# Kernel optimization log

Measured on AMD Instinct MI355X. Metric: run time of the kernel, lower is better.

Reference implementation:

```python
import jax, jax.numpy as jnp
import numpy as np

DIM, HEADS, DHEAD, CTX_DIM, DFF = 1280, 20, 64, 768, 5120
EPS = 1e-5
SCALE = DHEAD ** -0.5


def layer_norm(x, g, b):
    mu = jnp.mean(x, axis=-1, keepdims=True)
    var = jnp.mean(jnp.square(x - mu), axis=-1, keepdims=True)
    return (x - mu) * jax.lax.rsqrt(var + EPS) * g + b


def cross_attention(x, ctx, wq, wk, wv, wo, bo):
    B, N, _ = x.shape
    M = ctx.shape[1]
    q = jnp.einsum('bne,ef->bnf', x, wq).reshape(B, N, HEADS, DHEAD).transpose(0, 2, 1, 3)
    k = jnp.einsum('bme,ef->bmf', ctx, wk).reshape(B, M, HEADS, DHEAD).transpose(0, 2, 1, 3)
    v = jnp.einsum('bme,ef->bmf', ctx, wv).reshape(B, M, HEADS, DHEAD).transpose(0, 2, 1, 3)
    scores = jnp.einsum('bhnd,bhmd->bhnm', q, k) * SCALE
    attn = jax.nn.softmax(scores, axis=-1)
    out = jnp.einsum('bhnm,bhmd->bhnd', attn, v)
    out = out.transpose(0, 2, 1, 3).reshape(B, N, HEADS * DHEAD)
    return jnp.einsum('bnf,fe->bne', out, wo) + bo


def geglu_ff(x, w1, b1, w2, b2):
    h = jnp.einsum('bne,ef->bnf', x, w1) + b1  # [B,N,2*DFF]
    a, gate = h[..., :DFF], h[..., DFF:]
    h = a * jax.nn.gelu(gate)
    return jnp.einsum('bnf,fe->bne', h, w2) + b2


def block_forward(x, context,
                  g1, be1, wq1, wk1, wv1, wo1, bo1,
                  g2, be2, wq2, wk2, wv2, wo2, bo2,
                  g3, be3, w_ff1, b_ff1, w_ff2, b_ff2):
    x = cross_attention(layer_norm(x, g1, be1), layer_norm(x, g1, be1), wq1, wk1, wv1, wo1, bo1) + x
    x = cross_attention(layer_norm(x, g2, be2), context, wq2, wk2, wv2, wo2, bo2) + x
    return geglu_ff(layer_norm(x, g3, be3), w_ff1, b_ff1, w_ff2, b_ff2) + x


def setup_inputs() -> dict:
    key = jax.random.key(0)
    ks = jax.random.split(key, 20)
    s = 0.02
    inner = HEADS * DHEAD
    return {
        'x': jax.random.normal(ks[0], (4, 1024, DIM), jnp.float32),
        'context': jax.random.normal(ks[1], (4, 77, CTX_DIM), jnp.float32),
        'g1': jnp.ones((DIM,), jnp.float32), 'be1': jnp.zeros((DIM,), jnp.float32),
        'wq1': jax.random.normal(ks[2], (DIM, inner), jnp.float32) * s,
        'wk1': jax.random.normal(ks[3], (DIM, inner), jnp.float32) * s,
        'wv1': jax.random.normal(ks[4], (DIM, inner), jnp.float32) * s,
        'wo1': jax.random.normal(ks[5], (inner, DIM), jnp.float32) * s,
        'bo1': jnp.zeros((DIM,), jnp.float32),
        'g2': jnp.ones((DIM,), jnp.float32), 'be2': jnp.zeros((DIM,), jnp.float32),
        'wq2': jax.random.normal(ks[6], (DIM, inner), jnp.float32) * s,
        'wk2': jax.random.normal(ks[7], (CTX_DIM, inner), jnp.float32) * s,
        'wv2': jax.random.normal(ks[8], (CTX_DIM, inner), jnp.float32) * s,
        'wo2': jax.random.normal(ks[9], (inner, DIM), jnp.float32) * s,
        'bo2': jnp.zeros((DIM,), jnp.float32),
        'g3': jnp.ones((DIM,), jnp.float32), 'be3': jnp.zeros((DIM,), jnp.float32),
        'w_ff1': jax.random.normal(ks[10], (DIM, 2 * DFF), jnp.float32) * s,
        'b_ff1': jnp.zeros((2 * DFF,), jnp.float32),
        'w_ff2': jax.random.normal(ks[11], (DFF, DIM), jnp.float32) * s,
        'b_ff2': jnp.zeros((DIM,), jnp.float32),
    }


def reference(x, context,
              g1, be1, wq1, wk1, wv1, wo1, bo1,
              g2, be2, wq2, wk2, wv2, wo2, bo2,
              g3, be3, w_ff1, b_ff1, w_ff2, b_ff2):
    return block_forward(x, context,
                         g1, be1, wq1, wk1, wv1, wo1, bo1,
                         g2, be2, wq2, wk2, wv2, wo2, bo2,
                         g3, be3, w_ff1, b_ff1, w_ff2, b_ff2)
```

## Files before the change

### kernel.cpp

```cpp
#include <hip/hip_runtime.h>

typedef unsigned short u16;
typedef __bf16 bf16x8 __attribute__((ext_vector_type(8)));
typedef float f32x4 __attribute__((ext_vector_type(4)));

static __device__ __forceinline__ float bf2f(u16 u) {
    union { unsigned int i; float f; } v; v.i = ((unsigned int)u) << 16; return v.f;
}
static __device__ __forceinline__ u16 f2bf(float f) {
    union { float f; unsigned int i; } v; v.f = f;
    unsigned int b = v.i;
    b += 0x7fffu + ((b >> 16) & 1u);
    return (u16)(b >> 16);
}
static __device__ __forceinline__ u16 ldbf(const void* p, size_t i, int isf32) {
    return isf32 ? f2bf(((const float*)p)[i]) : ((const u16*)p)[i];
}
static __device__ __forceinline__ float ldf(const void* p, size_t i, int isf32) {
    return isf32 ? ((const float*)p)[i] : bf2f(((const u16*)p)[i]);
}
static __device__ __forceinline__ void glds16(const u16* g, u16* l) {
    __builtin_amdgcn_global_load_lds(
        (const __attribute__((address_space(1))) unsigned int*)g,
        (__attribute__((address_space(3))) unsigned int*)l,
        16, 0, 0);
}

__global__ __launch_bounds__(256) void k_detect(const u16* __restrict__ xu, int* __restrict__ flag) {
    u16 v = xu[threadIdx.x * 2];
    int e = (v >> 7) & 0xFF;
    int sane = (e >= 87 && e <= 133) ? 1 : 0;
    int total = __syncthreads_count(sane);
    if (threadIdx.x == 0) flag[0] = (total < 192) ? 1 : 0;
}

__global__ __launch_bounds__(256) void k_b2f(const void* __restrict__ in, float* __restrict__ out, int n,
                                             const int* __restrict__ flagp) {
    int isf32 = *flagp;
    int i = blockIdx.x * 256 + threadIdx.x;
    if (i < n) out[i] = ldf(in, i, isf32);
}

__global__ __launch_bounds__(256) void k_cvt(const void* __restrict__ in, u16* __restrict__ out, int n,
                                             const int* __restrict__ flagp) {
    int isf32 = *flagp;
    int i = blockIdx.x * 256 + threadIdx.x;
    if (i < n) out[i] = ldbf(in, i, isf32);
}

__global__ __launch_bounds__(256) void k_transpose(const void* __restrict__ W, u16* __restrict__ Wt,
                                                   int K, int N, const int* __restrict__ flagp) {
    int isf32 = *flagp;
    __shared__ u16 T[32][33];
    int k0 = blockIdx.x * 32, n0 = blockIdx.y * 32;
    int tid = threadIdx.x;
    int c = tid & 31, rr = tid >> 5;
    #pragma unroll
    for (int j = 0; j < 4; ++j) {
        int k = rr + j * 8;
        T[k][c] = ldbf(W, (size_t)(k0 + k) * N + n0 + c, isf32);
    }
    __syncthreads();
    #pragma unroll
    for (int j = 0; j < 4; ++j) {
        int n = rr + j * 8;
        Wt[(size_t)(n0 + n) * K + k0 + c] = T[c][n];
    }
}

__global__ __launch_bounds__(256) void k_layernorm(const float* __restrict__ X, const void* __restrict__ G,
                                                   const void* __restrict__ Bb, u16* __restrict__ Y, int D,
                                                   const int* __restrict__ flagp) {
    int isf32 = *flagp;
    int row = blockIdx.x;
    const float* xr = X + (size_t)row * D;
    float s = 0.f, s2 = 0.f;
    for (int i = threadIdx.x; i < D; i += 256) { float v = xr[i]; s += v; s2 += v * v; }
    #pragma unroll
    for (int off = 32; off; off >>= 1) { s += __shfl_down(s, off); s2 += __shfl_down(s2, off); }
    __shared__ float rs[4], rs2[4];
    __shared__ float stat[2];
    int w = threadIdx.x >> 6;
    if ((threadIdx.x & 63) == 0) { rs[w] = s; rs2[w] = s2; }
    __syncthreads();
    if (threadIdx.x == 0) {
        float ts = rs[0] + rs[1] + rs[2] + rs[3];
        float ts2 = rs2[0] + rs2[1] + rs2[2] + rs2[3];
        float mu = ts / D;
        float var = ts2 / D - mu * mu;
        stat[0] = mu; stat[1] = rsqrtf(var + 1e-5f);
    }
    __syncthreads();
    float mu = stat[0], rstd = stat[1];
    u16* yr = Y + (size_t)row * D;
    for (int i = threadIdx.x; i < D; i += 256) {
        yr[i] = f2bf((xr[i] - mu) * rstd * ldf(G, i, isf32) + ldf(Bb, i, isf32));
    }
}

template <int EPI>
__global__ __launch_bounds__(512, 2) void k_gemm8(const u16* __restrict__ A, const u16* __restrict__ Bt,
                                                  void* __restrict__ Cout, const void* __restrict__ bias,
                                                  int M, int N, int K, const int* __restrict__ flagp) {
    __shared__ __align__(16) u16 sm[65536];
    const int tid = threadIdx.x;
    const int w = tid >> 6;
    const int lane = tid & 63;
    const int quad = lane >> 4, r = lane & 15;
    const int wm = w >> 2, wn = w & 3;
    const int row0 = blockIdx.x * 256, col0 = blockIdx.y * 256;
    const int NT = K >> 6;

    const u16* aP[2][2];
    const u16* bP[2][2];
    #pragma unroll
    for (int j = 0; j < 2; ++j) {
        int c = tid + w * 64 + j * 64;
        int rj = c >> 3;
        int qe = (c & 7) ^ (rj & 7);
        #pragma unroll
        for (int h = 0; h < 2; ++h) {
            int gr = h * 128 + rj;
            aP[h][j] = A + (size_t)(row0 + gr) * K + qe * 8;
            int n = col0 + gr;
            int m = (EPI == 1) ? (((n >> 4) & 1) * 5120 + (n >> 5) * 16 + (n & 15)) : n;
            bP[h][j] = Bt + (size_t)m * K + qe * 8;
        }
    }
    auto stageA = [&](int h, int t) {
        u16* base = sm + (t & 1) * 32768 + h * 8192 + w * 1024;
        glds16(aP[h][0] + t * 64, base);
        glds16(aP[h][1] + t * 64, base + 512);
    };
    auto stageB = [&](int h, int t) {
        u16* base = sm + (t & 1) * 32768 + 16384 + h * 8192 + w * 1024;
        glds16(bP[h][0] + t * 64, base);
        glds16(bP[h][1] + t * 64, base + 512);
    };

    stageA(0, 0); stageB(0, 0); stageA(1, 0); stageB(1, 0);
    if (NT > 1) {
        stageA(0, 1); stageB(0, 1);
        asm volatile("s_waitcnt vmcnt(4)" ::: "memory");
    } else {
        asm volatile("s_waitcnt vmcnt(0)" ::: "memory");
    }
    __builtin_amdgcn_s_barrier();

    f32x4 acc[2][2][4][2] = {};
    const int xq = r & 7;
    for (int t = 0; t < NT; ++t) {
        const int Ab = (t & 1) * 32768;
        const int Bb = Ab + 16384;
        #pragma unroll
        for (int qp = 0; qp < 4; ++qp) {
            const int qm = qp >> 1, qn = qp & 1;
            bf16x8 af[4][2], bf[2][2];
            #pragma unroll
            for (int i = 0; i < 4; ++i) {
                int ar = qm * 128 + wm * 64 + i * 16 + r;
                #pragma unroll
                for (int ks = 0; ks < 2; ++ks)
                    af[i][ks] = *(const bf16x8*)(sm + Ab + ar * 64 + (((ks * 4 + quad) ^ xq) * 8));
            }
            #pragma unroll
            for (int g = 0; g < 2; ++g) {
                int br = qn * 128 + wn * 32 + g * 16 + r;
                #pragma unroll
                for (int ks = 0; ks < 2; ++ks)
                    bf[g][ks] = *(const bf16x8*)(sm + Bb + br * 64 + (((ks * 4 + quad) ^ xq) * 8));
            }
            if (qp == 0)      { if (t + 1 < NT) stageA(1, t + 1); }
            else if (qp == 1) { if (t + 1 < NT) stageB(1, t + 1); }
            else if (qp == 2) { if (t + 2 < NT) stageA(0, t + 2); }
            else              { if (t + 2 < NT) stageB(0, t + 2); }
            __builtin_amdgcn_s_barrier();
            asm volatile("s_waitcnt lgkmcnt(0)" ::: "memory");
            __builtin_amdgcn_sched_barrier(0);
            __builtin_amdgcn_s_setprio(1);
            #pragma unroll
            for (int ks = 0; ks < 2; ++ks)
                #pragma unroll
                for (int i = 0; i < 4; ++i)
                    #pragma unroll
                    for (int g = 0; g < 2; ++g)
                        acc[qm][qn][i][g] = __builtin_amdgcn_mfma_f32_16x16x32_bf16(
                            af[i][ks], bf[g][ks], acc[qm][qn][i][g], 0, 0, 0);
            __builtin_amdgcn_s_setprio(0);
            if (qp == 3) {
                if (t + 2 < NT) asm volatile("s_waitcnt vmcnt(4)" ::: "memory");
                else            asm volatile("s_waitcnt vmcnt(0)" ::: "memory");
            }
            __builtin_amdgcn_s_barrier();
        }
    }

    if (EPI == 0) {
        u16* C = (u16*)Cout;
        #pragma unroll
        for (int qm = 0; qm < 2; ++qm) {
            #pragma unroll
            for (int qn = 0; qn < 2; ++qn) {
                #pragma unroll
                for (int i = 0; i < 4; ++i) {
                    int grow = row0 + qm * 128 + wm * 64 + i * 16 + quad * 4;
                    #pragma unroll
                    for (int g = 0; g < 2; ++g) {
                        int gcol = col0 + qn * 128 + wn * 32 + g * 16 + r;
                        #pragma unroll
                        for (int t4 = 0; t4 < 4; ++t4)
                            C[(size_t)(grow + t4) * N + gcol] = f2bf(acc[qm][qn][i][g][t4]);
                    }
                }
            }
        }
    } else {
        const int isf32 = *flagp;
        u16* C = (u16*)Cout;
        #pragma unroll
        for (int qm = 0; qm < 2; ++qm) {
            #pragma unroll
            for (int qn = 0; qn < 2; ++qn) {
                int ncb = col0 + qn * 128 + wn * 32;
                int oc = (ncb >> 1) + r;
                float bva = ldf(bias, oc, isf32);
                float bvu = ldf(bias, 5120 + oc, isf32);
                #pragma unroll
                for (int i = 0; i < 4; ++i) {
                    int grow = row0 + qm * 128 + wm * 64 + i * 16 + quad * 4;
                    #pragma unroll
                    for (int t4 = 0; t4 < 4; ++t4) {
                        float a = acc[qm][qn][i][0][t4] + bva;
                        float u = acc[qm][qn][i][1][t4] + bvu;
                        float z2 = 1.5957691216f * (u + 0.044715f * u * u * u);
                        float gl = u * __builtin_amdgcn_rcpf(1.f + __expf(-z2));
                        C[(size_t)(grow + t4) * 5120 + oc] = f2bf(a * gl);
                    }
                }
            }
        }
    }
}

template <int EPI>
__global__ __launch_bounds__(256) void k_gemm_t(const u16* __restrict__ A, const u16* __restrict__ Bt,
                                                void* __restrict__ Cout, float* __restrict__ Rf,
                                                const void* __restrict__ bias,
                                                int M, int N, int K, const int* __restrict__ flagp) {
    int isf32 = *flagp;
    __shared__ __align__(16) u16 As[4096];
    __shared__ __align__(16) u16 Bs[4096];
    int tid = threadIdx.x;
    int row0 = blockIdx.x * 128, col0 = blockIdx.y * 128;
    int wave = tid >> 6, lane = tid & 63;
    int wm = (wave >> 1) * 64, wn = (wave & 1) * 64;
    int quad = lane >> 4, r = lane & 15;
    int c0 = wave * 64 + lane, c1 = 256 + c0;
    int ar0 = c0 >> 2, aq0 = (c0 & 3) ^ ((ar0 >> 1) & 3);
    int ar1 = c1 >> 2, aq1 = (c1 & 3) ^ ((ar1 >> 1) & 3);
    const u16* Ag0 = A + (size_t)min(row0 + ar0, M - 1) * K + aq0 * 8;
    const u16* Ag1 = A + (size_t)min(row0 + ar1, M - 1) * K + aq1 * 8;
    const u16* Bg0 = Bt + (size_t)(col0 + ar0) * K + aq0 * 8;
    const u16* Bg1 = Bt + (size_t)(col0 + ar1) * K + aq1 * 8;
    u16* lA0 = As + wave * 512;
    u16* lA1 = As + 2048 + wave * 512;
    u16* lB0 = Bs + wave * 512;
    u16* lB1 = Bs + 2048 + wave * 512;
    f32x4 acc[4][4] = {};
    for (int k0 = 0; k0 < K; k0 += 32) {
        __syncthreads();
        glds16(Ag0 + k0, lA0);
        glds16(Ag1 + k0, lA1);
        glds16(Bg0 + k0, lB0);
        glds16(Bg1 + k0, lB1);
        __syncthreads();
        bf16x8 af[4], bfv[4];
        #pragma unroll
        for (int i = 0; i < 4; ++i) {
            int row = wm + i * 16 + r;
            af[i] = *(const bf16x8*)(As + (row * 4 + (quad ^ ((row >> 1) & 3))) * 8);
        }
        #pragma unroll
        for (int g = 0; g < 4; ++g) {
            int row = wn + g * 16 + r;
            bfv[g] = *(const bf16x8*)(Bs + (row * 4 + (quad ^ ((row >> 1) & 3))) * 8);
        }
        #pragma unroll
        for (int i = 0; i < 4; ++i)
            #pragma unroll
            for (int g = 0; g < 4; ++g)
                acc[i][g] = __builtin_amdgcn_mfma_f32_16x16x32_bf16(af[i], bfv[g], acc[i][g], 0, 0, 0);
    }
    #pragma unroll
    for (int i = 0; i < 4; ++i) {
        int grow = row0 + wm + i * 16 + quad * 4;
        if (grow >= M) continue;
        #pragma unroll
        for (int g = 0; g < 4; ++g) {
            int gcol = col0 + wn + g * 16 + r;
            float bv = (EPI == 2) ? ldf(bias, gcol, isf32) : 0.f;
            #pragma unroll
            for (int t = 0; t < 4; ++t) {
                float v = acc[i][g][t];
                size_t off = (size_t)(grow + t) * N + gcol;
                if (EPI == 0) ((u16*)Cout)[off] = f2bf(v);
                else Rf[off] += v + bv;
            }
        }
    }
}

__global__ __launch_bounds__(256) void k_geglu_t(const u16* __restrict__ A, const u16* __restrict__ Bt,
                                                 const void* __restrict__ bias, u16* __restrict__ Out,
                                                 int M, int K, const int* __restrict__ flagp) {
    const int Nout = 5120;
    int isf32 = *flagp;
    __shared__ __align__(16) u16 As[4096];
    __shared__ __align__(16) u16 Bs[4096];
    int tid = threadIdx.x;
    int row0 = blockIdx.x * 128, col0 = blockIdx.y * 64;
    int wave = tid >> 6, lane = tid & 63;
    int quad = lane >> 4, r = lane & 15;
    int c0 = wave * 64 + lane, c1 = 256 + c0;
    int ar0 = c0 >> 2, aq0 = (c0 & 3) ^ ((ar0 >> 1) & 3);
    int ar1 = c1 >> 2, aq1 = (c1 & 3) ^ ((ar1 >> 1) & 3);
    const u16* Ag0 = A + (size_t)min(row0 + ar0, M - 1) * K + aq0 * 8;
    const u16* Ag1 = A + (size_t)min(row0 + ar1, M - 1) * K + aq1 * 8;
    const u16* Bg0 = Bt + (size_t)((ar0 >> 6) * Nout + col0 + (ar0 & 63)) * K + aq0 * 8;
    const u16* Bg1 = Bt + (size_t)((ar1 >> 6) * Nout + col0 + (ar1 & 63)) * K + aq1 * 8;
    u16* lA0 = As + wave * 512;
    u16* lA1 = As + 2048 + wave * 512;
    u16* lB0 = Bs + wave * 512;
    u16* lB1 = Bs + 2048 + wave * 512;
    f32x4 acc[2][2][4] = {};
    for (int k0 = 0; k0 < K; k0 += 32) {
        __syncthreads();
        glds16(Ag0 + k0, lA0);
        glds16(Ag1 + k0, lA1);
        glds16(Bg0 + k0, lB0);
        glds16(Bg1 + k0, lB1);
        __syncthreads();
        bf16x8 af[2], bv[2][4];
        #pragma unroll
        for (int i = 0; i < 2; ++i) {
            int row = wave * 32 + i * 16 + r;
            af[i] = *(const bf16x8*)(As + (row * 4 + (quad ^ ((row >> 1) & 3))) * 8);
        }
        #pragma unroll
        for (int p = 0; p < 2; ++p)
            #pragma unroll
            for (int g = 0; g < 4; ++g) {
                int row = p * 64 + g * 16 + r;
                bv[p][g] = *(const bf16x8*)(Bs + (row * 4 + (quad ^ ((row >> 1) & 3))) * 8);
            }
        #pragma unroll
        for (int p = 0; p < 2; ++p)
            #pragma unroll
            for (int i = 0; i < 2; ++i)
                #pragma unroll
                for (int g = 0; g < 4; ++g)
                    acc[p][i][g] = __builtin_amdgcn_mfma_f32_16x16x32_bf16(af[i], bv[p][g], acc[p][i][g], 0, 0, 0);
    }
    #pragma unroll
    for (int i = 0; i < 2; ++i) {
        int grow = row0 + wave * 32 + i * 16 + quad * 4;
        #pragma unroll
        for (int g = 0; g < 4; ++g) {
            int gcol = col0 + g * 16 + r;
            float bva = ldf(bias, gcol, isf32);
            float bvu = ldf(bias, Nout + gcol, isf32);
            #pragma unroll
            for (int t = 0; t < 4; ++t) {
                float a = acc[0][i][g][t] + bva;
                float u = acc[1][i][g][t] + bvu;
                float z2 = 1.5957691216f * (u + 0.044715f * u * u * u);
                float gl = u * __builtin_amdgcn_rcpf(1.f + __expf(-z2));
                Out[(size_t)(grow + t) * Nout + gcol] = f2bf(a * gl);
            }
        }
    }
}

template <int EPI, bool AEXT>
__global__ __launch_bounds__(256) void k_gemm(const void* __restrict__ A, const void* __restrict__ B,
                                              void* __restrict__ Cout, float* __restrict__ Rf,
                                              const void* __restrict__ bias,
                                              int M, int N, int K, const int* __restrict__ flagp) {
    int isf32 = *flagp;
    __shared__ u16 As[64][40];
    __shared__ u16 Bs[64][40];
    int tid = threadIdx.x;
    int row0 = blockIdx.x * 64, col0 = blockIdx.y * 64;
    int wave = tid >> 6, lane = tid & 63;
    int wm = (wave >> 1) * 32, wn = (wave & 1) * 32;
    int quad = lane >> 4, r = lane & 15;
    int arow = tid >> 2, akk = (tid & 3) * 8;
    int bnl = tid & 63, bkk = (tid >> 6) * 8;
    int garow = row0 + arow;
    f32x4 acc[2][2] = {};
    for (int k0 = 0; k0 < K; k0 += 32) {
        uint4 aval = {0u, 0u, 0u, 0u};
        if (garow < M) {
            if (AEXT && isf32) {
                const float* Af = (const float*)A;
                u16 t[8];
                #pragma unroll
                for (int j = 0; j < 8; ++j) t[j] = f2bf(Af[(size_t)garow * K + k0 + akk + j]);
                aval = *(uint4*)t;
            } else {
                aval = *(const uint4*)((const u16*)A + (size_t)garow * K + k0 + akk);
            }
        }
        u16 btmp[8];
        #pragma unroll
        for (int j = 0; j < 8; ++j) btmp[j] = ldbf(B, (size_t)(k0 + bkk + j) * N + col0 + bnl, isf32);
        __syncthreads();
        *(uint4*)(&As[arow][akk]) = aval;
        *(uint4*)(&Bs[bnl][bkk]) = *(uint4*)btmp;
        __syncthreads();
        bf16x8 a0 = *(const bf16x8*)(&As[wm + r][quad * 8]);
        bf16x8 a1 = *(const bf16x8*)(&As[wm + 16 + r][quad * 8]);
        bf16x8 b0 = *(const bf16x8*)(&Bs[wn + r][quad * 8]);
        bf16x8 b1 = *(const bf16x8*)(&Bs[wn + 16 + r][quad * 8]);
        acc[0][0] = __builtin_amdgcn_mfma_f32_16x16x32_bf16(a0, b0, acc[0][0], 0, 0, 0);
        acc[0][1] = __builtin_amdgcn_mfma_f32_16x16x32_bf16(a0, b1, acc[0][1], 0, 0, 0);
        acc[1][0] = __builtin_amdgcn_mfma_f32_16x16x32_bf16(a1, b0, acc[1][0], 0, 0, 0);
        acc[1][1] = __builtin_amdgcn_mfma_f32_16x16x32_bf16(a1, b1, acc[1][1], 0, 0, 0);
    }
    #pragma unroll
    for (int i = 0; i < 2; ++i)
        #pragma unroll
        for (int jn = 0; jn < 2; ++jn)
            #pragma unroll
            for (int t = 0; t < 4; ++t) {
                int grow = row0 + wm + i * 16 + quad * 4 + t;
                int gcol = col0 + wn + jn * 16 + r;
                if (grow >= M) continue;
                float v = acc[i][jn][t];
                size_t off = (size_t)grow * N + gcol;
                if (EPI == 0) {
                    ((u16*)Cout)[off] = f2bf(v);
                } else if (EPI == 2) {
                    Rf[off] += v + ldf(bias, gcol, isf32);
                } else {
                    ((float*)Cout)[off] = v + ldf(bias, gcol, isf32) + Rf[off];
                }
            }
}

__global__ __launch_bounds__(256) void k_gemm_geglu(const u16* __restrict__ A, const void* __restrict__ B,
                                                    const void* __restrict__ bias, u16* __restrict__ Out,
                                                    int M, int Nout, int K, int ldb,
                                                    const int* __restrict__ flagp) {
    int isf32 = *flagp;
    __shared__ u16 As[64][40];
    __shared__ u16 Bs[64][40];
    int tid = threadIdx.x;
    int row0 = blockIdx.x * 64, col0 = blockIdx.y * 64;
    int wave = tid >> 6, lane = tid & 63;
    int wm = (wave >> 1) * 32, wn = (wave & 1) * 32;
    int quad = lane >> 4, r = lane & 15;
    int arow = tid >> 2, akk = (tid & 3) * 8;
    int bnl = tid & 63, bkk = (tid >> 6) * 8;
    int garow = row0 + arow;
    f32x4 acc[2][2][2] = {};
    for (int p = 0; p < 2; ++p) {
        for (int k0 = 0; k0 < K; k0 += 32) {
            uint4 aval = {0u, 0u, 0u, 0u};
            if (garow < M) aval = *(const uint4*)(A + (size_t)garow * K + k0 + akk);
            u16 btmp[8];
            #pragma unroll
            for (int j = 0; j < 8; ++j)
                btmp[j] = ldbf(B, (size_t)(k0 + bkk + j) * ldb + p * Nout + col0 + bnl, isf32);
            __syncthreads();
            *(uint4*)(&As[arow][akk]) = aval;
            *(uint4*)(&Bs[bnl][bkk]) = *(uint4*)btmp;
            __syncthreads();
            bf16x8 a0 = *(const bf16x8*)(&As[wm + r][quad * 8]);
            bf16x8 a1 = *(const bf16x8*)(&As[wm + 16 + r][quad * 8]);
            bf16x8 b0 = *(const bf16x8*)(&Bs[wn + r][quad * 8]);
            bf16x8 b1 = *(const bf16x8*)(&Bs[wn + 16 + r][quad * 8]);
            acc[p][0][0] = __builtin_amdgcn_mfma_f32_16x16x32_bf16(a0, b0, acc[p][0][0], 0, 0, 0);
            acc[p][0][1] = __builtin_amdgcn_mfma_f32_16x16x32_bf16(a0, b1, acc[p][0][1], 0, 0, 0);
            acc[p][1][0] = __builtin_amdgcn_mfma_f32_16x16x32_bf16(a1, b0, acc[p][1][0], 0, 0, 0);
            acc[p][1][1] = __builtin_amdgcn_mfma_f32_16x16x32_bf16(a1, b1, acc[p][1][1], 0, 0, 0);
        }
    }
    #pragma unroll
    for (int i = 0; i < 2; ++i)
        #pragma unroll
        for (int jn = 0; jn < 2; ++jn)
            #pragma unroll
            for (int t = 0; t < 4; ++t) {
                int grow = row0 + wm + i * 16 + quad * 4 + t;
                int gcol = col0 + wn + jn * 16 + r;
                if (grow >= M) continue;
                float a = acc[0][i][jn][t] + ldf(bias, gcol, isf32);
                float u = acc[1][i][jn][t] + ldf(bias, Nout + gcol, isf32);
                float th = tanhf(0.7978845608f * (u + 0.044715f * u * u * u));
                float gl = 0.5f * u * (1.f + th);
                Out[(size_t)grow * Nout + gcol] = f2bf(a * gl);
            }
}

__global__ __launch_bounds__(256) void k_attn_flash(const u16* __restrict__ Q, const u16* __restrict__ K,
                                                    const u16* __restrict__ V, u16* __restrict__ O,
                                                    int N, int Mkv, int H, int ldq, int ldkv, int ldo) {
    __shared__ u16 Sp[4][16][40];
    __shared__ u16 VT[64][40];
    int nt = N / 64;
    int qt = blockIdx.x % nt;
    int bh = blockIdx.x / nt;
    int h = bh % H, b = bh / H;
    int tid = threadIdx.x, wave = tid >> 6, lane = tid & 63;
    int quad = lane >> 4, r = lane & 15;
    int q0 = qt * 64 + wave * 16;

    const u16* qbase = Q + ((size_t)(b * N + q0 + r)) * ldq + h * 64;
    bf16x8 aq0 = *(const bf16x8*)(qbase + quad * 8);
    bf16x8 aq1 = *(const bf16x8*)(qbase + 32 + quad * 8);

    f32x4 accO[4] = {};
    float m_i[4] = {-1e30f, -1e30f, -1e30f, -1e30f};
    float l_i[4] = {0.f, 0.f, 0.f, 0.f};

    int vkv = tid & 31, vdg = tid >> 5;

    for (int kv0 = 0; kv0 < Mkv; kv0 += 32) {
        int kr0 = min(kv0 + r, Mkv - 1);
        int kr1 = min(kv0 + 16 + r, Mkv - 1);
        const u16* kb0 = K + ((size_t)(b * Mkv + kr0)) * ldkv + h * 64;
        const u16* kb1 = K + ((size_t)(b * Mkv + kr1)) * ldkv + h * 64;
        bf16x8 bk00 = *(const bf16x8*)(kb0 + quad * 8);
        bf16x8 bk01 = *(const bf16x8*)(kb0 + 32 + quad * 8);
        bf16x8 bk10 = *(const bf16x8*)(kb1 + quad * 8);
        bf16x8 bk11 = *(const bf16x8*)(kb1 + 32 + quad * 8);
        int vrow = min(kv0 + vkv, Mkv - 1);
        uint4 vv = *(const uint4*)(V + ((size_t)(b * Mkv + vrow)) * ldkv + h * 64 + vdg * 8);

        __syncthreads();
        VT[vdg * 8 + 0][vkv] = (u16)(vv.x);
        VT[vdg * 8 + 1][vkv] = (u16)(vv.x >> 16);
        VT[vdg * 8 + 2][vkv] = (u16)(vv.y);
        VT[vdg * 8 + 3][vkv] = (u16)(vv.y >> 16);
        VT[vdg * 8 + 4][vkv] = (u16)(vv.z);
        VT[vdg * 8 + 5][vkv] = (u16)(vv.z >> 16);
        VT[vdg * 8 + 6][vkv] = (u16)(vv.w);
        VT[vdg * 8 + 7][vkv] = (u16)(vv.w >> 16);
        __syncthreads();

        f32x4 s0 = {}, s1 = {};
        s0 = __builtin_amdgcn_mfma_f32_16x16x32_bf16(aq0, bk00, s0, 0, 0, 0);
        s0 = __builtin_amdgcn_mfma_f32_16x16x32_bf16(aq1, bk01, s0, 0, 0, 0);
        s1 = __builtin_amdgcn_mfma_f32_16x16x32_bf16(aq0, bk10, s1, 0, 0, 0);
        s1 = __builtin_amdgcn_mfma_f32_16x16x32_bf16(aq1, bk11, s1, 0, 0, 0);
        bool mask0 = (kv0 + r) >= Mkv;
        bool mask1 = (kv0 + 16 + r) >= Mkv;

        #pragma unroll
        for (int t = 0; t < 4; ++t) {
            float a = mask0 ? -1e30f : s0[t] * 0.125f;
            float c = mask1 ? -1e30f : s1[t] * 0.125f;
            float mx = fmaxf(a, c);
            mx = fmaxf(mx, __shfl_xor(mx, 1));
            mx = fmaxf(mx, __shfl_xor(mx, 2));
            mx = fmaxf(mx, __shfl_xor(mx, 4));
            mx = fmaxf(mx, __shfl_xor(mx, 8));
            float mn = fmaxf(m_i[t], mx);
            float alpha = __expf(m_i[t] - mn);
            float p0 = __expf(a - mn);
            float p1 = __expf(c - mn);
            float ps = p0 + p1;
            ps += __shfl_xor(ps, 1);
            ps += __shfl_xor(ps, 2);
            ps += __shfl_xor(ps, 4);
            ps += __shfl_xor(ps, 8);
            l_i[t] = l_i[t] * alpha + ps;
            m_i[t] = mn;
            accO[0][t] *= alpha; accO[1][t] *= alpha; accO[2][t] *= alpha; accO[3][t] *= alpha;
            Sp[wave][quad * 4 + t][r] = f2bf(p0);
            Sp[wave][quad * 4 + t][16 + r] = f2bf(p1);
        }

        bf16x8 ap = *(const bf16x8*)(&Sp[wave][r][quad * 8]);
        #pragma unroll
        for (int g = 0; g < 4; ++g) {
            bf16x8 bvv = *(const bf16x8*)(&VT[g * 16 + r][quad * 8]);
            accO[g] = __builtin_amdgcn_mfma_f32_16x16x32_bf16(ap, bvv, accO[g], 0, 0, 0);
        }
    }

    u16* ob = O + ((size_t)(b * N + q0)) * ldo + h * 64;
    #pragma unroll
    for (int t = 0; t < 4; ++t) {
        float inv = 1.f / l_i[t];
        #pragma unroll
        for (int g = 0; g < 4; ++g)
            ob[(size_t)(quad * 4 + t) * ldo + g * 16 + r] = f2bf(accO[g][t] * inv);
    }
}

extern "C" void kernel_launch(void* const* d_in, const int* in_sizes, int n_in,
                              void* d_out, int out_size, void* d_ws, size_t ws_size,
                              hipStream_t stream) {
    const void* x    = d_in[0];
    const void* ctx  = d_in[1];
    const void* g1   = d_in[2];
    const void* be1  = d_in[3];
    const void* wq1  = d_in[4];
    const void* wk1  = d_in[5];
    const void* wv1  = d_in[6];
    const void* wo1  = d_in[7];
    const void* bo1  = d_in[8];
    const void* g2   = d_in[9];
    const void* be2  = d_in[10];
    const void* wq2  = d_in[11];
    const void* wk2  = d_in[12];
    const void* wv2  = d_in[13];
    const void* wo2  = d_in[14];
    const void* bo2  = d_in[15];
    const void* g3   = d_in[16];
    const void* be3  = d_in[17];
    const void* wff1 = d_in[18];
    const void* bff1 = d_in[19];
    const void* wff2 = d_in[20];
    const void* bff2 = d_in[21];

    const int BT = 4096, D = 1280;
    dim3 blk(256);
    char* ws = (char*)d_ws;

    const size_t NEED_FAST = 117393664;
    if (ws_size >= NEED_FAST) {
        int*   flag   = (int*)(ws);
        u16* lnout    = (u16*)(ws + 256);
        u16* qkv      = (u16*)(ws + 10486016);
        u16* attnout  = (u16*)(ws + 10486016 + 31457280);
        u16* gbuf     = (u16*)(ws + 10486016);
        u16* ctxb     = (u16*)(ws + 52429056);
        u16* kv2      = (u16*)(ws + 52902144);
        u16* wqkv1t   = (u16*)(ws + 54479104);
        u16* wo1t     = (u16*)(ws + 64309504);
        u16* wq2t     = (u16*)(ws + 67586304);
        u16* wkv2t    = (u16*)(ws + 70863104);
        u16* wo2t     = (u16*)(ws + 74795264);
        u16* wff1t    = (u16*)(ws + 78072064);
        u16* wff2t    = (u16*)(ws + 104286464);
        float* xres   = (float*)d_out;

        k_detect<<<dim3(1), blk, 0, stream>>>((const u16*)x, flag);
        k_b2f<<<dim3((BT * D + 255) / 256), blk, 0, stream>>>(x, xres, BT * D, flag);
        k_transpose<<<dim3(40, 40), blk, 0, stream>>>(wq1, wqkv1t, 1280, 1280, flag);
        k_transpose<<<dim3(40, 40), blk, 0, stream>>>(wk1, wqkv1t + 1280 * 1280, 1280, 1280, flag);
        k_transpose<<<dim3(40, 40), blk, 0, stream>>>(wv1, wqkv1t + 2 * 1280 * 1280, 1280, 1280, flag);
        k_transpose<<<dim3(40, 40), blk, 0, stream>>>(wo1, wo1t, 1280, 1280, flag);
        k_transpose<<<dim3(40, 40), blk, 0, stream>>>(wq2, wq2t, 1280, 1280, flag);
        k_transpose<<<dim3(24, 40), blk, 0, stream>>>(wk2, wkv2t, 768, 1280, flag);
        k_transpose<<<dim3(24, 40), blk, 0, stream>>>(wv2, wkv2t + 1280 * 768, 768, 1280, flag);
        k_transpose<<<dim3(40, 40), blk, 0, stream>>>(wo2, wo2t, 1280, 1280, flag);
        k_transpose<<<dim3(40, 320), blk, 0, stream>>>(wff1, wff1t, 1280, 10240, flag);
        k_transpose<<<dim3(160, 40), blk, 0, stream>>>(wff2, wff2t, 5120, 1280, flag);
        k_cvt<<<dim3((308 * 768 + 255) / 256), blk, 0, stream>>>(ctx, ctxb, 308 * 768, flag);
        k_layernorm<<<dim3(BT), blk, 0, stream>>>(xres, g1, be1, lnout, D, flag);
        k_gemm8<0><<<dim3(16, 15), dim3(512), 0, stream>>>(lnout, wqkv1t, qkv, nullptr, BT, 3840, D, flag);
        k_attn_flash<<<dim3(16 * 80), blk, 0, stream>>>(qkv, qkv + 1280, qkv + 2560, attnout,
                                                        1024, 1024, 20, 3840, 3840, 1280);
        k_gemm_t<2><<<dim3(32, 10), blk, 0, stream>>>(attnout, wo1t, nullptr, xres, bo1, BT, D, D, flag);
        k_layernorm<<<dim3(BT), blk, 0, stream>>>(xres, g2, be2, lnout, D, flag);
        k_gemm_t<0><<<dim3(32, 10), blk, 0, stream>>>(lnout, wq2t, qkv, nullptr, nullptr, BT, D, D, flag);
        k_gemm_t<0><<<dim3(3, 20), blk, 0, stream>>>(ctxb, wkv2t, kv2, nullptr, nullptr, 308, 2560, 768, flag);
        k_attn_flash<<<dim3(16 * 80), blk, 0, stream>>>(qkv, kv2, kv2 + 1280, attnout,
                                                        1024, 77, 20, 1280, 2560, 1280);
        k_gemm_t<2><<<dim3(32, 10), blk, 0, stream>>>(attnout, wo2t, nullptr, xres, bo2, BT, D, D, flag);
        k_layernorm<<<dim3(BT), blk, 0, stream>>>(xres, g3, be3, lnout, D, flag);
        k_gemm8<1><<<dim3(16, 40), dim3(512), 0, stream>>>(lnout, wff1t, gbuf, bff1, BT, 10240, D, flag);
        k_gemm_t<2><<<dim3(32, 10), blk, 0, stream>>>(gbuf, wff2t, nullptr, xres, bff2, BT, D, 5120, flag);
    } else {
        int*   flag    = (int*)(ws);
        float* xres    = (float*)(ws + 256);
        u16* lnout     = (u16*)(ws + 20971776);
        u16* q         = (u16*)(ws + 31457536);
        u16* kbuf      = (u16*)(ws + 41943296);
        u16* vbuf      = (u16*)(ws + 52429056);
        u16* attnout   = (u16*)(ws + 62914816);
        u16* k2        = (u16*)(ws + 73400576);
        u16* v2        = (u16*)(ws + 74189056);
        u16* gbuf      = (u16*)(ws + 31457536);

        dim3 g_gemm(64, 20);
        dim3 g_kv(5, 20);
        dim3 g_attn(16 * 80);

        k_detect<<<dim3(1), blk, 0, stream>>>((const u16*)x, flag);
        k_b2f<<<dim3((BT * D + 255) / 256), blk, 0, stream>>>(x, xres, BT * D, flag);
        k_layernorm<<<dim3(BT), blk, 0, stream>>>(xres, g1, be1, lnout, D, flag);
        k_gemm<0, false><<<g_gemm, blk, 0, stream>>>(lnout, wq1, q, nullptr, nullptr, BT, D, D, flag);
        k_gemm<0, false><<<g_gemm, blk, 0, stream>>>(lnout, wk1, kbuf, nullptr, nullptr, BT, D, D, flag);
        k_gemm<0, false><<<g_gemm, blk, 0, stream>>>(lnout, wv1, vbuf, nullptr, nullptr, BT, D, D, flag);
        k_attn_flash<<<g_attn, blk, 0, stream>>>(q, kbuf, vbuf, attnout, 1024, 1024, 20, 1280, 1280, 1280);
        k_gemm<2, false><<<g_gemm, blk, 0, stream>>>(attnout, wo1, nullptr, xres, bo1, BT, D, D, flag);
        k_layernorm<<<dim3(BT), blk, 0, stream>>>(xres, g2, be2, lnout, D, flag);
        k_gemm<0, false><<<g_gemm, blk, 0, stream>>>(lnout, wq2, q, nullptr, nullptr, BT, D, D, flag);
        k_gemm<0, true><<<g_kv, blk, 0, stream>>>(ctx, wk2, k2, nullptr, nullptr, 308, D, 768, flag);
        k_gemm<0, true><<<g_kv, blk, 0, stream>>>(ctx, wv2, v2, nullptr, nullptr, 308, D, 768, flag);
        k_attn_flash<<<g_attn, blk, 0, stream>>>(q, k2, v2, attnout, 1024, 77, 20, 1280, 1280, 1280);
        k_gemm<2, false><<<g_gemm, blk, 0, stream>>>(attnout, wo2, nullptr, xres, bo2, BT, D, D, flag);
        k_layernorm<<<dim3(BT), blk, 0, stream>>>(xres, g3, be3, lnout, D, flag);
        k_gemm_geglu<<<dim3(64, 80), blk, 0, stream>>>(lnout, wff1, bff1, gbuf, BT, 5120, D, 10240, flag);
        k_gemm<3, false><<<g_gemm, blk, 0, stream>>>(gbuf, wff2, d_out, xres, bff2, BT, D, 5120, flag);
    }
}
```

Baseline: 875.9 us.

## Reuse LDS fragments across quadrants and prefetch next A fragment in GEMM loop

The GEMM main loop now visits its four output quadrants in the order (0,0),(0,1),(1,1),(1,0), so each A and B register fragment is read from LDS once per K-step and reused across two quadrants. Before, every quadrant reloaded both fragments. The first A fragment for the next K-step is read at the end of the current step, after the barrier. This cuts LDS read traffic by about half but keeps more fragment registers live, which may raise register pressure and lower occupancy. It also reorders the barrier and wait placement around the async global-to-LDS staging, so correctness depends on that ordering.

```diff
diff --git a/kernel.cpp b/kernel.cpp
--- a/kernel.cpp
+++ b/kernel.cpp
@@ -138,6 +138,39 @@
         glds16(bP[h][1] + t * 64, base + 512);
     };
 
+    f32x4 acc[2][2][4][2] = {};
+    const int xq = r & 7;
+    bf16x8 afA[4][2], afB[4][2], bf0[2][2], bf1[2][2];
+
+    auto readA = [&](bf16x8 (&dst)[4][2], int Ab, int half) {
+        #pragma unroll
+        for (int i = 0; i < 4; ++i) {
+            int ar = half * 128 + wm * 64 + i * 16 + r;
+            #pragma unroll
+            for (int ks = 0; ks < 2; ++ks)
+                dst[i][ks] = *(const bf16x8*)(sm + Ab + ar * 64 + (((ks * 4 + quad) ^ xq) * 8));
+        }
+    };
+    auto readB = [&](bf16x8 (&dst)[2][2], int Bb, int half) {
+        #pragma unroll
+        for (int g = 0; g < 2; ++g) {
+            int br = half * 128 + wn * 32 + g * 16 + r;
+            #pragma unroll
+            for (int ks = 0; ks < 2; ++ks)
+                dst[g][ks] = *(const bf16x8*)(sm + Bb + br * 64 + (((ks * 4 + quad) ^ xq) * 8));
+        }
+    };
+    auto domfma = [&](int qm, int qn, bf16x8 (&a)[4][2], bf16x8 (&b)[2][2]) {
+        #pragma unroll
+        for (int ks = 0; ks < 2; ++ks)
+            #pragma unroll
+            for (int i = 0; i < 4; ++i)
+                #pragma unroll
+                for (int g = 0; g < 2; ++g)
+                    acc[qm][qn][i][g] = __builtin_amdgcn_mfma_f32_16x16x32_bf16(
+                        a[i][ks], b[g][ks], acc[qm][qn][i][g], 0, 0, 0);
+    };
+
     stageA(0, 0); stageB(0, 0); stageA(1, 0); stageB(1, 0);
     if (NT > 1) {
         stageA(0, 1); stageB(0, 1);
@@ -146,53 +179,48 @@
         asm volatile("s_waitcnt vmcnt(0)" ::: "memory");
     }
     __builtin_amdgcn_s_barrier();
-
-    f32x4 acc[2][2][4][2] = {};
-    const int xq = r & 7;
+    readA(afA, 0, 0);
+
     for (int t = 0; t < NT; ++t) {
         const int Ab = (t & 1) * 32768;
         const int Bb = Ab + 16384;
-        #pragma unroll
-        for (int qp = 0; qp < 4; ++qp) {
-            const int qm = qp >> 1, qn = qp & 1;
-            bf16x8 af[4][2], bf[2][2];
-            #pragma unroll
-            for (int i = 0; i < 4; ++i) {
-                int ar = qm * 128 + wm * 64 + i * 16 + r;
-                #pragma unroll
-                for (int ks = 0; ks < 2; ++ks)
-                    af[i][ks] = *(const bf16x8*)(sm + Ab + ar * 64 + (((ks * 4 + quad) ^ xq) * 8));
-            }
-            #pragma unroll
-            for (int g = 0; g < 2; ++g) {
-                int br = qn * 128 + wn * 32 + g * 16 + r;
-                #pragma unroll
-                for (int ks = 0; ks < 2; ++ks)
-                    bf[g][ks] = *(const bf16x8*)(sm + Bb + br * 64 + (((ks * 4 + quad) ^ xq) * 8));
-            }
-            if (qp == 0)      { if (t + 1 < NT) stageA(1, t + 1); }
-            else if (qp == 1) { if (t + 1 < NT) stageB(1, t + 1); }
-            else if (qp == 2) { if (t + 2 < NT) stageA(0, t + 2); }
-            else              { if (t + 2 < NT) stageB(0, t + 2); }
-            __builtin_amdgcn_s_barrier();
-            asm volatile("s_waitcnt lgkmcnt(0)" ::: "memory");
-            __builtin_amdgcn_sched_barrier(0);
-            __builtin_amdgcn_s_setprio(1);
-            #pragma unroll
-            for (int ks = 0; ks < 2; ++ks)
-                #pragma unroll
-                for (int i = 0; i < 4; ++i)
-                    #pragma unroll
-                    for (int g = 0; g < 2; ++g)
-                        acc[qm][qn][i][g] = __builtin_amdgcn_mfma_f32_16x16x32_bf16(
-                            af[i][ks], bf[g][ks], acc[qm][qn][i][g], 0, 0, 0);
-            __builtin_amdgcn_s_setprio(0);
-            if (qp == 3) {
-                if (t + 2 < NT) asm volatile("s_waitcnt vmcnt(4)" ::: "memory");
-                else            asm volatile("s_waitcnt vmcnt(0)" ::: "memory");
-            }
-            __builtin_amdgcn_s_barrier();
-        }
+        const int Ab1 = ((t + 1) & 1) * 32768;
+        readB(bf0, Bb, 0);
+        if (t + 1 < NT) stageA(1, t + 1);
+        __builtin_amdgcn_s_barrier();
+        asm volatile("s_waitcnt lgkmcnt(0)" ::: "memory");
+        __builtin_amdgcn_sched_barrier(0);
+        __builtin_amdgcn_s_setprio(1);
+        domfma(0, 0, afA, bf0);
+        __builtin_amdgcn_s_setprio(0);
+        __builtin_amdgcn_s_barrier();
+        readB(bf1, Bb, 1);
+        if (t + 1 < NT) stageB(1, t + 1);
+        __builtin_amdgcn_s_barrier();
+        asm volatile("s_waitcnt lgkmcnt(0)" ::: "memory");
+        __builtin_amdgcn_sched_barrier(0);
+        __builtin_amdgcn_s_setprio(1);
+        domfma(0, 1, afA, bf1);
+        __builtin_amdgcn_s_setprio(0);
+        __builtin_amdgcn_s_barrier();
+        readA(afB, Ab, 1);
+        if (t + 2 < NT) stageA(0, t + 2);
+        __builtin_amdgcn_s_barrier();
+        asm volatile("s_waitcnt lgkmcnt(0)" ::: "memory");
+        __builtin_amdgcn_sched_barrier(0);
+        __builtin_amdgcn_s_setprio(1);
+        domfma(1, 1, afB, bf1);
+        __builtin_amdgcn_s_setprio(0);
+        __builtin_amdgcn_s_barrier();
+        if (t + 2 < NT) stageB(0, t + 2);
+        __builtin_amdgcn_s_barrier();
+        __builtin_amdgcn_s_setprio(1);
+        domfma(1, 0, afB, bf0);
+        __builtin_amdgcn_s_setprio(0);
+        if (t + 2 < NT) asm volatile("s_waitcnt vmcnt(4)" ::: "memory");
+        else            asm volatile("s_waitcnt vmcnt(0)" ::: "memory");
+        __builtin_amdgcn_s_barrier();
+        if (t + 1 < NT) readA(afA, Ab1, 0);
     }
 
     if (EPI == 0) {
```

Result: faster. 856.4 us (-2.2%).
